# Kernel optimization log

Hardware: AMD Instinct MI355X
Metric: run time of the kernel (lower is better)

## Reference

```python
import math
import jax, jax.numpy as jnp
import numpy as np

HEAD_DIM = 64
N_HEAD = 8
INIT_SIZE = 1200  # -> 1201 embeddings, origin_shift = 601


def rel_sinusoidal_pos_embed(seq_len, dim=HEAD_DIM):
    """Matches RelativeSinusoidalPositionalEmbedding(dim, padding_idx=0, init_size=1200)."""
    num = INIT_SIZE + 1  # 1201
    half = dim // 2
    inv_freq = jnp.exp(jnp.arange(half, dtype=jnp.float32) * -(math.log(10000.0) / (half - 1)))
    pos = jnp.arange(-(num // 2), num // 2, dtype=jnp.float32)  # -601 .. 599 (1201 values)
    ang = pos[:, None] * inv_freq[None, :]                      # [num, half]
    w = jnp.concatenate([jnp.sin(ang), jnp.cos(ang)], axis=1)   # [num, dim]
    w = w.at[0].set(0.0)  # padding_idx row zeroed
    origin_shift = num // 2 + 1  # 601
    idx = jnp.arange(-seq_len, seq_len) + origin_shift          # [2L]
    return w[idx]                                               # [2L, dim]


def _shift(BD):
    # BD: [b, n, L, 2L] -> [b, n, L, L] (Transformer-XL skew trick)
    b, n, L, _ = BD.shape
    BD = jnp.pad(BD, ((0, 0), (0, 0), (0, 0), (0, 1)))  # [b,n,L,2L+1]
    BD = BD.reshape(b, n, 2 * L + 1, L)[:, :, :-1].reshape(b, n, L, 2 * L)
    return BD[:, :, :, L:]


def _transpose_shift(E):
    # E: [b, n, L, 2L] -> [b, n, L, L]
    b, n, L, _ = E.shape
    E = jnp.pad(E, ((0, 0), (0, 0), (0, 0), (0, 1))).reshape(b, n, 2 * L + 1, L)
    idx = jnp.arange(L) * 2 + 1
    return jnp.swapaxes(E[:, :, idx, :], -1, -2)


def setup_inputs() -> dict:
    key = jax.random.key(0)
    k1, k2, k3, k4 = jax.random.split(key, 4)
    B, L, D = 8, 512, 512
    x = jax.random.normal(k1, (B, L, D), dtype=jnp.float32)
    mask = jnp.ones((B, L), dtype=jnp.int32)
    W_qkv = jax.random.normal(k2, (D, 3 * D), dtype=jnp.float32) * (1.0 / math.sqrt(D))
    r_r_bias = jax.random.normal(k3, (N_HEAD, HEAD_DIM), dtype=jnp.float32) * 0.1
    r_w_bias = jax.random.normal(k4, (N_HEAD, HEAD_DIM), dtype=jnp.float32) * 0.1
    return {"x": x, "mask": mask, "W_qkv": W_qkv, "r_r_bias": r_r_bias, "r_w_bias": r_w_bias}


def reference(x, mask, W_qkv, r_r_bias, r_w_bias):
    B, L, D = x.shape
    scale = math.sqrt(HEAD_DIM)
    pos = rel_sinusoidal_pos_embed(L)  # [2L, head_dim], detached constant

    qkv = x @ W_qkv  # [B, L, 3D]
    q, k, v = jnp.split(qkv, 3, axis=-1)
    q = q.reshape(B, L, N_HEAD, HEAD_DIM).transpose(0, 2, 1, 3)  # [B,H,L,d]
    k = k.reshape(B, L, N_HEAD, HEAD_DIM).transpose(0, 2, 1, 3)
    v = v.reshape(B, L, N_HEAD, HEAD_DIM).transpose(0, 2, 1, 3)

    rw_head_q = q + r_r_bias[None, :, None, :]
    AC = jnp.einsum('bnqd,bnkd->bnqk', rw_head_q, k)              # [B,H,L,L]
    D_ = jnp.einsum('nd,ld->nl', r_w_bias, pos)[None, :, None, :] # [1,H,1,2L]
    B_ = jnp.einsum('bnqd,ld->bnql', q, pos)                      # [B,H,L,2L]
    E_ = jnp.einsum('bnqd,ld->bnql', k, pos)                      # [B,H,L,2L]

    BDE = _shift(B_ + D_) + _transpose_shift(E_)                  # [B,H,L,L]
    attn = (AC + BDE) / scale
    attn = jnp.where(mask[:, None, None, :] == 0, -jnp.inf, attn)
    attn = jax.nn.softmax(attn, axis=-1)

    out = jnp.matmul(attn, v)                                     # [B,H,L,d]
    return out.transpose(0, 2, 1, 3).reshape(B, L, D)
```

## Files before the change

kernel.cpp:

```cpp
#include <hip/hip_runtime.h>
#include <hip/hip_bf16.h>
#include <math.h>

#define LSEQ 512
#define DDIM 192

typedef __attribute__((ext_vector_type(8))) short s16x8;
typedef __attribute__((ext_vector_type(4))) float f32x4;
typedef unsigned short ushort_t;
typedef unsigned int uint_t;

#define MFMA16(a, b, c) __builtin_amdgcn_mfma_f32_16x16x32_bf16(a, b, c, 0, 0, 0)

__device__ __forceinline__ ushort_t f2b(float f) {
  union { float f; uint_t u; } v; v.f = f;
  uint_t r = (v.u + 0x7FFFu + ((v.u >> 16) & 1u)) >> 16;
  return (ushort_t)r;
}

typedef const __attribute__((address_space(1))) void g_void_t;
typedef __attribute__((address_space(3))) void lds_void_t;
__device__ __forceinline__ void load_lds16(const void* g, void* l) {
  __builtin_amdgcn_global_load_lds((g_void_t*)g, (lds_void_t*)l, 16, 0, 0);
}

__device__ __forceinline__ size_t kswz(size_t row, int d) {
  return row * DDIM + (size_t)((d & 0x1C7) | ((((d >> 3) & 7) ^ ((int)row & 7)) << 3));
}

__global__ void cast_all(const float* __restrict__ x, const float* __restrict__ W,
                         ushort_t* __restrict__ xb, ushort_t* __restrict__ Wt) {
  __shared__ float tile[32][33];
  const int id = blockIdx.x;
  if (id < 1024) {
    const int i = (id * 256 + threadIdx.x) * 8;
    const int row = i >> 9, k = i & 511;
    float4 a = *(const float4*)(x + i);
    float4 b = *(const float4*)(x + i + 4);
    uint4 o;
    o.x = (uint_t)f2b(a.x) | ((uint_t)f2b(a.y) << 16);
    o.y = (uint_t)f2b(a.z) | ((uint_t)f2b(a.w) << 16);
    o.z = (uint_t)f2b(b.x) | ((uint_t)f2b(b.y) << 16);
    o.w = (uint_t)f2b(b.z) | ((uint_t)f2b(b.w) << 16);
    const int dst = row * 512 + (k & 448) + (((((k >> 3) & 7) ^ (row & 7))) << 3);
    *(uint4*)(xb + dst) = o;
  } else {
    const int wid = id - 1024;
    const int tx = threadIdx.x & 31, ty = threadIdx.x >> 5;
    const int k0 = (wid & 15) * 32, n0 = (wid >> 4) * 32;
#pragma unroll
    for (int i = 0; i < 4; ++i)
      tile[ty + i * 8][tx] = W[(size_t)(k0 + ty + i * 8) * 1536 + n0 + tx];
    __syncthreads();
#pragma unroll
    for (int i = 0; i < 4; ++i) {
      const int n = n0 + ty + i * 8, k = k0 + tx;
      Wt[(size_t)n * 512 + (k & 448) + ((((k >> 3) & 7) ^ (n & 7)) << 3) + (k & 7)] =
          f2b(tile[tx][ty + i * 8]);
    }
  }
}

__global__ __launch_bounds__(256, 2) void qkv_gemm(
    const ushort_t* __restrict__ xb, const ushort_t* __restrict__ Wt,
    const float* __restrict__ rr, const float* __restrict__ rw,
    ushort_t* __restrict__ Qt, ushort_t* __restrict__ Kt, ushort_t* __restrict__ Vt) {
  __shared__ __align__(16) ushort_t ldsA[2][128 * 64];
  __shared__ __align__(16) ushort_t ldsB[2][128 * 64];
  const int tid = threadIdx.x;
  const int w = tid >> 6, lane = tid & 63, lo = lane & 15, hi = lane >> 4;
  const int wm = w >> 1, wn = w & 1;
  const int id = blockIdx.x;
  const int mp = id & 31, np = id >> 5;
  const int m0 = mp * 128, n0 = np * 128;

  f32x4 acc[4][4];
  const f32x4 zero4 = {0.f, 0.f, 0.f, 0.f};
#pragma unroll
  for (int i = 0; i < 4; ++i)
#pragma unroll
    for (int j = 0; j < 4; ++j) acc[i][j] = zero4;

  const char* asrc = (const char*)xb + (size_t)m0 * 1024;
  const char* bsrc = (const char*)Wt + (size_t)n0 * 1024;

#define STAGE_QKV(buf, ks)                                                     \
  {                                                                            \
    char* la = (char*)&ldsA[buf][0];                                           \
    char* lb = (char*)&ldsB[buf][0];                                           \
    _Pragma("unroll") for (int it = 0; it < 4; ++it) {                         \
      const int X = it * 4096 + tid * 16;                                      \
      load_lds16(asrc + (size_t)(X >> 7) * 1024 + (ks) * 128 + (X & 127),      \
                 la + X);                                                      \
      load_lds16(bsrc + (size_t)(X >> 7) * 1024 + (ks) * 128 + (X & 127),      \
                 lb + X);                                                      \
    }                                                                          \
  }

  STAGE_QKV(0, 0);
  for (int ks = 0; ks < 8; ++ks) {
    const int cur = ks & 1;
    __syncthreads();
    if (ks < 7) STAGE_QKV(cur ^ 1, ks + 1);
    const char* Ab = (const char*)&ldsA[cur][0];
    const char* Bb = (const char*)&ldsB[cur][0];
#pragma unroll
    for (int kh = 0; kh < 2; ++kh) {
      const int sw = ((kh * 4 + hi) ^ (lo & 7)) << 4;
      s16x8 a[4], bf[4];
#pragma unroll
      for (int i = 0; i < 4; ++i)
        a[i] = *(const s16x8*)(Ab + (wm * 64 + i * 16 + lo) * 128 + sw);
#pragma unroll
      for (int j = 0; j < 4; ++j)
        bf[j] = *(const s16x8*)(Bb + (wn * 64 + j * 16 + lo) * 128 + sw);
#pragma unroll
      for (int i = 0; i < 4; ++i)
#pragma unroll
        for (int j = 0; j < 4; ++j)
          acc[i][j] = MFMA16(a[i], bf[j], acc[i][j]);
    }
  }

  const int gn0 = n0 + wn * 64;
  const int sect = gn0 >> 9;
  const int h = (gn0 >> 6) & 7;
  const int mrow0 = m0 + wm * 64;

  if (sect == 2) {
#pragma unroll
    for (int i = 0; i < 4; ++i) {
      const int m16 = mrow0 + i * 16;
      const int b = m16 >> 9;
      const int l0 = (m16 + hi * 4) & 511;
#pragma unroll
      for (int j = 0; j < 4; ++j) {
        ushort4 pk;
        pk.x = f2b(acc[i][j][0]); pk.y = f2b(acc[i][j][1]);
        pk.z = f2b(acc[i][j][2]); pk.w = f2b(acc[i][j][3]);
        *(ushort4*)&Vt[(((size_t)b * 8 + h) * 64 + j * 16 + lo) * 512 + l0] = pk;
      }
    }
  } else if (sect == 0) {
#pragma unroll
    for (int p = 0; p < 2; ++p) {
      const int hf = p * 16 + lo;
      const float rrs = rr[h * 64 + hf], rrc = rr[h * 64 + 32 + hf];
      const float rws = rw[h * 64 + hf], rwc = rw[h * 64 + 32 + hf];
      const float fq = __expf(-(float)hf * 0.29710775393472f);
      float sfr, cfr;
      __sincosf(fq, &sfr, &cfr);
#pragma unroll
      for (int i = 0; i < 4; ++i)
#pragma unroll
        for (int r = 0; r < 4; ++r) {
          const int m = mrow0 + i * 16 + hi * 4 + r;
          const int l = m & 511;
          const size_t base = (((size_t)(m >> 9) * 8 + h) * 512 + l) * DDIM;
          float s0, c0;
          __sincosf((float)l * fq, &s0, &c0);
          const float s1 = s0 * cfr + c0 * sfr;
          const float c1 = c0 * cfr - s0 * sfr;
          const float vs = acc[i][p][r], vc = acc[i][p + 2][r];
          const float qs = (vs + rws) * 0.125f, qc = (vc + rwc) * 0.125f;
          Qt[base + hf]       = f2b((vs + rrs) * 0.125f);
          Qt[base + 32 + hf]  = f2b((vc + rrc) * 0.125f);
          Qt[base + 64 + hf]  = f2b(qs * c0 + qc * s0);
          Qt[base + 96 + hf]  = f2b(qc * c0 - qs * s0);
          Qt[base + 128 + hf] = f2b(0.125f * s1);
          Qt[base + 160 + hf] = f2b(0.125f * c1);
        }
    }
  } else {
#pragma unroll
    for (int p = 0; p < 2; ++p) {
      const int hf = p * 16 + lo;
      const float fq = __expf(-(float)hf * 0.29710775393472f);
      float sfr, cfr;
      __sincosf(fq, &sfr, &cfr);
#pragma unroll
      for (int i = 0; i < 4; ++i)
#pragma unroll
        for (int r = 0; r < 4; ++r) {
          const int m = mrow0 + i * 16 + hi * 4 + r;
          const int l = m & 511;
          const size_t row = ((size_t)(m >> 9) * 8 + h) * 512 + l;
          float s0, c0;
          __sincosf((float)l * fq, &s0, &c0);
          const float s1 = s0 * cfr + c0 * sfr;
          const float c1 = c0 * cfr - s0 * sfr;
          const float ks_ = acc[i][p][r], kc_ = acc[i][p + 2][r];
          Kt[kswz(row, hf)]       = f2b(ks_);
          Kt[kswz(row, 32 + hf)]  = f2b(kc_);
          Kt[kswz(row, 64 + hf)]  = f2b(s1);
          Kt[kswz(row, 96 + hf)]  = f2b(c1);
          Kt[kswz(row, 128 + hf)] = f2b(ks_ * c0 + kc_ * s0);
          Kt[kswz(row, 160 + hf)] = f2b(kc_ * c0 - ks_ * s0);
        }
    }
  }
}

__global__ __launch_bounds__(256, 2) void attn_kernel(
    const ushort_t* __restrict__ Qt, const ushort_t* __restrict__ Kt,
    const ushort_t* __restrict__ Vt, const int* __restrict__ mask,
    float* __restrict__ out) {
  __shared__ __align__(16) ushort_t ldsK[2][64 * DDIM];
  __shared__ __align__(16) ushort_t P[4][16][72];

  const int tid = threadIdx.x;
  const int w = tid >> 6;
  const int lane = tid & 63, lo = lane & 15, hi = lane >> 4;
  const int id = blockIdx.x;
  const int bh = id & 63, qg = id >> 6;
  const int b = bh >> 3, h = bh & 7;
  const int q0 = qg * 64 + w * 16;
  const size_t qrow0 = (size_t)bh * LSEQ + q0;

  s16x8 qf[6];
#pragma unroll
  for (int ks = 0; ks < 6; ++ks)
    qf[ks] = *(const s16x8*)(Qt + (qrow0 + lo) * DDIM + ks * 32 + hi * 8);

  const f32x4 zero4 = {0.f, 0.f, 0.f, 0.f};
  f32x4 o[4];
#pragma unroll
  for (int j = 0; j < 4; ++j) o[j] = zero4;
  float mrun = -3.0e38f, lrun = 0.f;

  const char* ksrc = (const char*)(Kt + (size_t)bh * LSEQ * DDIM);
  const ushort_t* vbase = Vt + ((size_t)bh * 64 + lo) * 512 + hi * 8;

#pragma unroll
  for (int it = 0; it < 6; ++it) {
    const int X = it * 4096 + tid * 16;
    load_lds16(ksrc + X, (char*)&ldsK[0][0] + X);
  }

  for (int kt = 0; kt < 8; ++kt) {
    const int cur = kt & 1;

    const int mk = mask[b * LSEQ + kt * 64 + lane];
    s16x8 vbf[2][4];
#pragma unroll
    for (int kh = 0; kh < 2; ++kh)
#pragma unroll
      for (int j = 0; j < 4; ++j)
        vbf[kh][j] = *(const s16x8*)(vbase + (size_t)j * 16 * 512 + kt * 64 + kh * 32);

    __syncthreads();
    if (kt < 7) {
      const char* s = ksrc + (kt + 1) * 24576;
      char* d = (char*)&ldsK[cur ^ 1][0];
#pragma unroll
      for (int it = 0; it < 6; ++it) {
        const int X = it * 4096 + tid * 16;
        load_lds16(s + X, d + X);
      }
    }

    f32x4 sf[4];
#pragma unroll
    for (int f = 0; f < 4; ++f) sf[f] = zero4;
    const char* kl = (const char*)&ldsK[cur][0];
    __builtin_amdgcn_s_setprio(1);
#pragma unroll
    for (int ks = 0; ks < 6; ++ks) {
      const int swb = ((ks * 4 + hi) ^ (lo & 7)) << 4;
#pragma unroll
      for (int f = 0; f < 4; ++f) {
        s16x8 ka = *(const s16x8*)(kl + (f * 16 + lo) * 384 + swb);
        sf[f] = MFMA16(ka, qf[ks], sf[f]);
      }
    }
    __builtin_amdgcn_s_setprio(0);

    if (__ballot(mk == 0) != 0ull) {
#pragma unroll
      for (int f = 0; f < 4; ++f)
#pragma unroll
        for (int r = 0; r < 4; ++r)
          if (__shfl(mk, f * 16 + hi * 4 + r) == 0) sf[f][r] = -3.0e38f;
    }

    float tm = fmaxf(fmaxf(sf[0][0], sf[0][1]), fmaxf(sf[0][2], sf[0][3]));
#pragma unroll
    for (int f = 1; f < 4; ++f)
      tm = fmaxf(tm, fmaxf(fmaxf(sf[f][0], sf[f][1]), fmaxf(sf[f][2], sf[f][3])));
    tm = fmaxf(tm, __shfl_xor(tm, 16));
    tm = fmaxf(tm, __shfl_xor(tm, 32));

    if (!__all(tm - mrun <= 8.0f)) {
      const float mnew = fmaxf(mrun, tm);
      const float corr = __expf(mrun - mnew);
      lrun *= corr;
      mrun = mnew;
      float cq[4];
#pragma unroll
      for (int r = 0; r < 4; ++r) cq[r] = __shfl(corr, hi * 4 + r);
#pragma unroll
      for (int j = 0; j < 4; ++j)
#pragma unroll
        for (int r = 0; r < 4; ++r) o[j][r] *= cq[r];
    }

    float ts = 0.f;
#pragma unroll
    for (int f = 0; f < 4; ++f)
#pragma unroll
      for (int r = 0; r < 4; ++r) {
        sf[f][r] = __expf(sf[f][r] - mrun);
        ts += sf[f][r];
      }
    ts += __shfl_xor(ts, 16);
    ts += __shfl_xor(ts, 32);
    lrun += ts;

#pragma unroll
    for (int f = 0; f < 4; ++f) {
      __hip_bfloat162 p0 = __float22bfloat162_rn(make_float2(sf[f][0], sf[f][1]));
      __hip_bfloat162 p1 = __float22bfloat162_rn(make_float2(sf[f][2], sf[f][3]));
      uint2 u;
      __builtin_memcpy(&u.x, &p0, 4);
      __builtin_memcpy(&u.y, &p1, 4);
      *(uint2*)&P[w][lo][f * 16 + hi * 4] = u;
    }

    __builtin_amdgcn_s_setprio(1);
#pragma unroll
    for (int kh = 0; kh < 2; ++kh) {
      s16x8 pa = *(const s16x8*)&P[w][lo][kh * 32 + hi * 8];
#pragma unroll
      for (int j = 0; j < 4; ++j)
        o[j] = MFMA16(pa, vbf[kh][j], o[j]);
    }
    __builtin_amdgcn_s_setprio(0);
  }

  float lq[4];
#pragma unroll
  for (int r = 0; r < 4; ++r) lq[r] = 1.0f / __shfl(lrun, hi * 4 + r);
#pragma unroll
  for (int j = 0; j < 4; ++j)
#pragma unroll
    for (int r = 0; r < 4; ++r)
      out[((size_t)b * LSEQ + q0 + hi * 4 + r) * 512 + h * 64 + j * 16 + lo] =
          o[j][r] * lq[r];
}

extern "C" void kernel_launch(void* const* d_in, const int* in_sizes, int n_in,
                              void* d_out, int out_size, void* d_ws, size_t ws_size,
                              hipStream_t stream) {
  const float* x    = (const float*)d_in[0];
  const int*   mask = (const int*)d_in[1];
  const float* W    = (const float*)d_in[2];
  const float* rr   = (const float*)d_in[3];
  const float* rw   = (const float*)d_in[4];
  float* out = (float*)d_out;

  char* ws = (char*)d_ws;
  ushort_t* xb = (ushort_t*)(ws);
  ushort_t* Wt = (ushort_t*)(ws + 4194304);
  ushort_t* Qt = (ushort_t*)(ws + 5767168);
  ushort_t* Kt = (ushort_t*)(ws + 18350080);
  ushort_t* Vt = (ushort_t*)(ws + 30932992);

  cast_all<<<1792, 256, 0, stream>>>(x, W, xb, Wt);
  qkv_gemm<<<384, 256, 0, stream>>>(xb, Wt, rr, rw, Qt, Kt, Vt);
  attn_kernel<<<512, 256, 0, stream>>>(Qt, Kt, Vt, mask, out);
}
```

Baseline: 53.35 us.

## Fuse cast, QKV GEMM and attention into one persistent kernel with grid barriers

Merges the three kernel launches into one 512-block persistent kernel. Its phases (cast, QKV GEMM, attention) are separated by atomic-counter grid barriers, and a tiny init kernel resets the counter each call. The aim is to remove launch gaps and inter-kernel drain/fill overhead. In exchange it relies on all 512 blocks being co-resident to avoid deadlock, adds spin-wait barrier costs, and uses a 64KB shared buffer that may limit occupancy. It also adds one extra small launch.

```diff
diff --git a/kernel.cpp b/kernel.cpp
--- a/kernel.cpp
+++ b/kernel.cpp
@@ -4,6 +4,7 @@
 
 #define LSEQ 512
 #define DDIM 192
+#define NBLK 512
 
 typedef __attribute__((ext_vector_type(8))) short s16x8;
 typedef __attribute__((ext_vector_type(4))) float f32x4;
@@ -28,66 +29,87 @@
   return row * DDIM + (size_t)((d & 0x1C7) | ((((d >> 3) & 7) ^ ((int)row & 7)) << 3));
 }
 
-__global__ void cast_all(const float* __restrict__ x, const float* __restrict__ W,
-                         ushort_t* __restrict__ xb, ushort_t* __restrict__ Wt) {
-  __shared__ float tile[32][33];
-  const int id = blockIdx.x;
-  if (id < 1024) {
-    const int i = (id * 256 + threadIdx.x) * 8;
-    const int row = i >> 9, k = i & 511;
-    float4 a = *(const float4*)(x + i);
-    float4 b = *(const float4*)(x + i + 4);
-    uint4 o;
-    o.x = (uint_t)f2b(a.x) | ((uint_t)f2b(a.y) << 16);
-    o.y = (uint_t)f2b(a.z) | ((uint_t)f2b(a.w) << 16);
-    o.z = (uint_t)f2b(b.x) | ((uint_t)f2b(b.y) << 16);
-    o.w = (uint_t)f2b(b.z) | ((uint_t)f2b(b.w) << 16);
-    const int dst = row * 512 + (k & 448) + (((((k >> 3) & 7) ^ (row & 7))) << 3);
-    *(uint4*)(xb + dst) = o;
-  } else {
-    const int wid = id - 1024;
-    const int tx = threadIdx.x & 31, ty = threadIdx.x >> 5;
-    const int k0 = (wid & 15) * 32, n0 = (wid >> 4) * 32;
+__global__ void init_bar(uint_t* c) { *c = 0u; }
+
+__device__ __forceinline__ void gridbar(uint_t* cnt, uint_t target) {
+  __syncthreads();
+  if (threadIdx.x == 0) {
+    __hip_atomic_fetch_add(cnt, 1u, __ATOMIC_ACQ_REL, __HIP_MEMORY_SCOPE_AGENT);
+    while (__hip_atomic_load(cnt, __ATOMIC_ACQUIRE, __HIP_MEMORY_SCOPE_AGENT) < target)
+      __builtin_amdgcn_s_sleep(2);
+  }
+  __syncthreads();
+}
+
+__global__ __launch_bounds__(256, 2) void mega(
+    const float* __restrict__ x, const float* __restrict__ W,
+    const float* __restrict__ rr, const float* __restrict__ rw,
+    const int* __restrict__ mask, float* __restrict__ out,
+    ushort_t* __restrict__ xb, ushort_t* __restrict__ Wt,
+    ushort_t* __restrict__ Qt, ushort_t* __restrict__ Kt,
+    ushort_t* __restrict__ Vt, uint_t* __restrict__ barcnt) {
+  __shared__ __align__(16) char smem[65536];
+  const int tid = threadIdx.x;
+  const int bid = blockIdx.x;
+
+  {
+    float (*tile)[33] = (float(*)[33])smem;
+    for (int unit = bid; unit < 1792; unit += NBLK) {
+      if (unit < 1024) {
+        const int i = (unit * 256 + tid) * 8;
+        const int row = i >> 9, k = i & 511;
+        float4 a = *(const float4*)(x + i);
+        float4 b = *(const float4*)(x + i + 4);
+        uint4 o;
+        o.x = (uint_t)f2b(a.x) | ((uint_t)f2b(a.y) << 16);
+        o.y = (uint_t)f2b(a.z) | ((uint_t)f2b(a.w) << 16);
+        o.z = (uint_t)f2b(b.x) | ((uint_t)f2b(b.y) << 16);
+        o.w = (uint_t)f2b(b.z) | ((uint_t)f2b(b.w) << 16);
+        const int dst = row * 512 + (k & 448) + (((((k >> 3) & 7) ^ (row & 7))) << 3);
+        *(uint4*)(xb + dst) = o;
+      } else {
+        const int wid = unit - 1024;
+        const int tx = tid & 31, ty = tid >> 5;
+        const int k0 = (wid & 15) * 32, n0 = (wid >> 4) * 32;
+        __syncthreads();
+#pragma unroll
+        for (int i = 0; i < 4; ++i)
+          tile[ty + i * 8][tx] = W[(size_t)(k0 + ty + i * 8) * 1536 + n0 + tx];
+        __syncthreads();
+#pragma unroll
+        for (int i = 0; i < 4; ++i) {
+          const int n = n0 + ty + i * 8, k = k0 + tx;
+          Wt[(size_t)n * 512 + (k & 448) + ((((k >> 3) & 7) ^ (n & 7)) << 3) + (k & 7)] =
+              f2b(tile[tx][ty + i * 8]);
+        }
+      }
+    }
+  }
+
+  gridbar(barcnt, NBLK);
+
+  if (bid < 384) {
+    ushort_t* ldsA = (ushort_t*)smem;
+    ushort_t* ldsB = (ushort_t*)(smem + 32768);
+    const int w = tid >> 6, lane = tid & 63, lo = lane & 15, hi = lane >> 4;
+    const int wm = w >> 1, wn = w & 1;
+    const int mp = bid & 31, np = bid >> 5;
+    const int m0 = mp * 128, n0 = np * 128;
+
+    f32x4 acc[4][4];
+    const f32x4 zero4 = {0.f, 0.f, 0.f, 0.f};
 #pragma unroll
     for (int i = 0; i < 4; ++i)
-      tile[ty + i * 8][tx] = W[(size_t)(k0 + ty + i * 8) * 1536 + n0 + tx];
-    __syncthreads();
-#pragma unroll
-    for (int i = 0; i < 4; ++i) {
-      const int n = n0 + ty + i * 8, k = k0 + tx;
-      Wt[(size_t)n * 512 + (k & 448) + ((((k >> 3) & 7) ^ (n & 7)) << 3) + (k & 7)] =
-          f2b(tile[tx][ty + i * 8]);
-    }
-  }
-}
-
-__global__ __launch_bounds__(256, 2) void qkv_gemm(
-    const ushort_t* __restrict__ xb, const ushort_t* __restrict__ Wt,
-    const float* __restrict__ rr, const float* __restrict__ rw,
-    ushort_t* __restrict__ Qt, ushort_t* __restrict__ Kt, ushort_t* __restrict__ Vt) {
-  __shared__ __align__(16) ushort_t ldsA[2][128 * 64];
-  __shared__ __align__(16) ushort_t ldsB[2][128 * 64];
-  const int tid = threadIdx.x;
-  const int w = tid >> 6, lane = tid & 63, lo = lane & 15, hi = lane >> 4;
-  const int wm = w >> 1, wn = w & 1;
-  const int id = blockIdx.x;
-  const int mp = id & 31, np = id >> 5;
-  const int m0 = mp * 128, n0 = np * 128;
-
-  f32x4 acc[4][4];
-  const f32x4 zero4 = {0.f, 0.f, 0.f, 0.f};
-#pragma unroll
-  for (int i = 0; i < 4; ++i)
-#pragma unroll
-    for (int j = 0; j < 4; ++j) acc[i][j] = zero4;
-
-  const char* asrc = (const char*)xb + (size_t)m0 * 1024;
-  const char* bsrc = (const char*)Wt + (size_t)n0 * 1024;
+#pragma unroll
+      for (int j = 0; j < 4; ++j) acc[i][j] = zero4;
+
+    const char* asrc = (const char*)xb + (size_t)m0 * 1024;
+    const char* bsrc = (const char*)Wt + (size_t)n0 * 1024;
 
 #define STAGE_QKV(buf, ks)                                                     \
   {                                                                            \
-    char* la = (char*)&ldsA[buf][0];                                           \
-    char* lb = (char*)&ldsB[buf][0];                                           \
+    char* la = (char*)ldsA + (buf) * 16384;                                    \
+    char* lb = (char*)ldsB + (buf) * 16384;                                    \
     _Pragma("unroll") for (int it = 0; it < 4; ++it) {                         \
       const int X = it * 4096 + tid * 16;                                      \
       load_lds16(asrc + (size_t)(X >> 7) * 1024 + (ks) * 128 + (X & 127),      \
@@ -97,255 +119,253 @@
     }                                                                          \
   }
 
-  STAGE_QKV(0, 0);
-  for (int ks = 0; ks < 8; ++ks) {
-    const int cur = ks & 1;
-    __syncthreads();
-    if (ks < 7) STAGE_QKV(cur ^ 1, ks + 1);
-    const char* Ab = (const char*)&ldsA[cur][0];
-    const char* Bb = (const char*)&ldsB[cur][0];
-#pragma unroll
-    for (int kh = 0; kh < 2; ++kh) {
-      const int sw = ((kh * 4 + hi) ^ (lo & 7)) << 4;
-      s16x8 a[4], bf[4];
-#pragma unroll
-      for (int i = 0; i < 4; ++i)
-        a[i] = *(const s16x8*)(Ab + (wm * 64 + i * 16 + lo) * 128 + sw);
-#pragma unroll
-      for (int j = 0; j < 4; ++j)
-        bf[j] = *(const s16x8*)(Bb + (wn * 64 + j * 16 + lo) * 128 + sw);
-#pragma unroll
-      for (int i = 0; i < 4; ++i)
+    STAGE_QKV(0, 0);
+    for (int ks = 0; ks < 8; ++ks) {
+      const int cur = ks & 1;
+      __syncthreads();
+      if (ks < 7) STAGE_QKV(cur ^ 1, ks + 1);
+      const char* Ab = (const char*)ldsA + cur * 16384;
+      const char* Bb = (const char*)ldsB + cur * 16384;
+#pragma unroll
+      for (int kh = 0; kh < 2; ++kh) {
+        const int sw = ((kh * 4 + hi) ^ (lo & 7)) << 4;
+        s16x8 a[4], bf[4];
+#pragma unroll
+        for (int i = 0; i < 4; ++i)
+          a[i] = *(const s16x8*)(Ab + (wm * 64 + i * 16 + lo) * 128 + sw);
 #pragma unroll
         for (int j = 0; j < 4; ++j)
-          acc[i][j] = MFMA16(a[i], bf[j], acc[i][j]);
-    }
-  }
-
-  const int gn0 = n0 + wn * 64;
-  const int sect = gn0 >> 9;
-  const int h = (gn0 >> 6) & 7;
-  const int mrow0 = m0 + wm * 64;
-
-  if (sect == 2) {
-#pragma unroll
-    for (int i = 0; i < 4; ++i) {
-      const int m16 = mrow0 + i * 16;
-      const int b = m16 >> 9;
-      const int l0 = (m16 + hi * 4) & 511;
-#pragma unroll
-      for (int j = 0; j < 4; ++j) {
-        ushort4 pk;
-        pk.x = f2b(acc[i][j][0]); pk.y = f2b(acc[i][j][1]);
-        pk.z = f2b(acc[i][j][2]); pk.w = f2b(acc[i][j][3]);
-        *(ushort4*)&Vt[(((size_t)b * 8 + h) * 64 + j * 16 + lo) * 512 + l0] = pk;
-      }
-    }
-  } else if (sect == 0) {
-#pragma unroll
-    for (int p = 0; p < 2; ++p) {
-      const int hf = p * 16 + lo;
-      const float rrs = rr[h * 64 + hf], rrc = rr[h * 64 + 32 + hf];
-      const float rws = rw[h * 64 + hf], rwc = rw[h * 64 + 32 + hf];
-      const float fq = __expf(-(float)hf * 0.29710775393472f);
-      float sfr, cfr;
-      __sincosf(fq, &sfr, &cfr);
-#pragma unroll
-      for (int i = 0; i < 4; ++i)
+          bf[j] = *(const s16x8*)(Bb + (wn * 64 + j * 16 + lo) * 128 + sw);
+#pragma unroll
+        for (int i = 0; i < 4; ++i)
+#pragma unroll
+          for (int j = 0; j < 4; ++j)
+            acc[i][j] = MFMA16(a[i], bf[j], acc[i][j]);
+      }
+    }
+
+    const int gn0 = n0 + wn * 64;
+    const int sect = gn0 >> 9;
+    const int h = (gn0 >> 6) & 7;
+    const int mrow0 = m0 + wm * 64;
+
+    if (sect == 2) {
+#pragma unroll
+      for (int i = 0; i < 4; ++i) {
+        const int m16 = mrow0 + i * 16;
+        const int b = m16 >> 9;
+        const int l0 = (m16 + hi * 4) & 511;
+#pragma unroll
+        for (int j = 0; j < 4; ++j) {
+          ushort4 pk;
+          pk.x = f2b(acc[i][j][0]); pk.y = f2b(acc[i][j][1]);
+          pk.z = f2b(acc[i][j][2]); pk.w = f2b(acc[i][j][3]);
+          *(ushort4*)&Vt[(((size_t)b * 8 + h) * 64 + j * 16 + lo) * 512 + l0] = pk;
+        }
+      }
+    } else if (sect == 0) {
+#pragma unroll
+      for (int p = 0; p < 2; ++p) {
+        const int hf = p * 16 + lo;
+        const float rrs = rr[h * 64 + hf], rrc = rr[h * 64 + 32 + hf];
+        const float rws = rw[h * 64 + hf], rwc = rw[h * 64 + 32 + hf];
+        const float fq = __expf(-(float)hf * 0.29710775393472f);
+        float sfr, cfr;
+        __sincosf(fq, &sfr, &cfr);
+#pragma unroll
+        for (int i = 0; i < 4; ++i)
+#pragma unroll
+          for (int r = 0; r < 4; ++r) {
+            const int m = mrow0 + i * 16 + hi * 4 + r;
+            const int l = m & 511;
+            const size_t base = (((size_t)(m >> 9) * 8 + h) * 512 + l) * DDIM;
+            float s0, c0;
+            __sincosf((float)l * fq, &s0, &c0);
+            const float s1 = s0 * cfr + c0 * sfr;
+            const float c1 = c0 * cfr - s0 * sfr;
+            const float vs = acc[i][p][r], vc = acc[i][p + 2][r];
+            const float qs = (vs + rws) * 0.125f, qc = (vc + rwc) * 0.125f;
+            Qt[base + hf]       = f2b((vs + rrs) * 0.125f);
+            Qt[base + 32 + hf]  = f2b((vc + rrc) * 0.125f);
+            Qt[base + 64 + hf]  = f2b(qs * c0 + qc * s0);
+            Qt[base + 96 + hf]  = f2b(qc * c0 - qs * s0);
+            Qt[base + 128 + hf] = f2b(0.125f * s1);
+            Qt[base + 160 + hf] = f2b(0.125f * c1);
+          }
+      }
+    } else {
+#pragma unroll
+      for (int p = 0; p < 2; ++p) {
+        const int hf = p * 16 + lo;
+        const float fq = __expf(-(float)hf * 0.29710775393472f);
+        float sfr, cfr;
+        __sincosf(fq, &sfr, &cfr);
+#pragma unroll
+        for (int i = 0; i < 4; ++i)
+#pragma unroll
+          for (int r = 0; r < 4; ++r) {
+            const int m = mrow0 + i * 16 + hi * 4 + r;
+            const int l = m & 511;
+            const size_t row = ((size_t)(m >> 9) * 8 + h) * 512 + l;
+            float s0, c0;
+            __sincosf((float)l * fq, &s0, &c0);
+            const float s1 = s0 * cfr + c0 * sfr;
+            const float c1 = c0 * cfr - s0 * sfr;
+            const float ks_ = acc[i][p][r], kc_ = acc[i][p + 2][r];
+            Kt[kswz(row, hf)]       = f2b(ks_);
+            Kt[kswz(row, 32 + hf)]  = f2b(kc_);
+            Kt[kswz(row, 64 + hf)]  = f2b(s1);
+            Kt[kswz(row, 96 + hf)]  = f2b(c1);
+            Kt[kswz(row, 128 + hf)] = f2b(ks_ * c0 + kc_ * s0);
+            Kt[kswz(row, 160 + hf)] = f2b(kc_ * c0 - ks_ * s0);
+          }
+      }
+    }
+  }
+
+  gridbar(barcnt, 2u * NBLK);
+
+  {
+    ushort_t* ldsK = (ushort_t*)smem;
+    ushort_t (*P)[16][72] = (ushort_t(*)[16][72])(smem + 49152);
+
+    const int w = tid >> 6;
+    const int lane = tid & 63, lo = lane & 15, hi = lane >> 4;
+    const int bh = bid & 63, qg = bid >> 6;
+    const int b = bh >> 3, h = bh & 7;
+    const int q0 = qg * 64 + w * 16;
+    const size_t qrow0 = (size_t)bh * LSEQ + q0;
+
+    s16x8 qf[6];
+#pragma unroll
+    for (int ks = 0; ks < 6; ++ks)
+      qf[ks] = *(const s16x8*)(Qt + (qrow0 + lo) * DDIM + ks * 32 + hi * 8);
+
+    const f32x4 zero4 = {0.f, 0.f, 0.f, 0.f};
+    f32x4 o[4];
+#pragma unroll
+    for (int j = 0; j < 4; ++j) o[j] = zero4;
+    float mrun = -3.0e38f, lrun = 0.f;
+
+    const char* ksrc = (const char*)(Kt + (size_t)bh * LSEQ * DDIM);
+    const ushort_t* vbase = Vt + ((size_t)bh * 64 + lo) * 512 + hi * 8;
+
+#pragma unroll
+    for (int it = 0; it < 6; ++it) {
+      const int X = it * 4096 + tid * 16;
+      load_lds16(ksrc + X, (char*)ldsK + X);
+    }
+
+    for (int kt = 0; kt < 8; ++kt) {
+      const int cur = kt & 1;
+
+      const int mk = mask[b * LSEQ + kt * 64 + lane];
+      s16x8 vbf[2][4];
+#pragma unroll
+      for (int kh = 0; kh < 2; ++kh)
+#pragma unroll
+        for (int j = 0; j < 4; ++j)
+          vbf[kh][j] = *(const s16x8*)(vbase + (size_t)j * 16 * 512 + kt * 64 + kh * 32);
+
+      __syncthreads();
+      if (kt < 7) {
+        const char* s = ksrc + (kt + 1) * 24576;
+        char* d = (char*)ldsK + (cur ^ 1) * 24576;
+#pragma unroll
+        for (int it = 0; it < 6; ++it) {
+          const int X = it * 4096 + tid * 16;
+          load_lds16(s + X, d + X);
+        }
+      }
+
+      f32x4 sf[4];
+#pragma unroll
+      for (int f = 0; f < 4; ++f) sf[f] = zero4;
+      const char* kl = (const char*)ldsK + cur * 24576;
+      __builtin_amdgcn_s_setprio(1);
+#pragma unroll
+      for (int ks = 0; ks < 6; ++ks) {
+        const int swb = ((ks * 4 + hi) ^ (lo & 7)) << 4;
+#pragma unroll
+        for (int f = 0; f < 4; ++f) {
+          s16x8 ka = *(const s16x8*)(kl + (f * 16 + lo) * 384 + swb);
+          sf[f] = MFMA16(ka, qf[ks], sf[f]);
+        }
+      }
+      __builtin_amdgcn_s_setprio(0);
+
+      if (__ballot(mk == 0) != 0ull) {
+#pragma unroll
+        for (int f = 0; f < 4; ++f)
+#pragma unroll
+          for (int r = 0; r < 4; ++r)
+            if (__shfl(mk, f * 16 + hi * 4 + r) == 0) sf[f][r] = -3.0e38f;
+      }
+
+      float tm = fmaxf(fmaxf(sf[0][0], sf[0][1]), fmaxf(sf[0][2], sf[0][3]));
+#pragma unroll
+      for (int f = 1; f < 4; ++f)
+        tm = fmaxf(tm, fmaxf(fmaxf(sf[f][0], sf[f][1]), fmaxf(sf[f][2], sf[f][3])));
+      tm = fmaxf(tm, __shfl_xor(tm, 16));
+      tm = fmaxf(tm, __shfl_xor(tm, 32));
+
+      if (!__all(tm - mrun <= 8.0f)) {
+        const float mnew = fmaxf(mrun, tm);
+        const float corr = __expf(mrun - mnew);
+        lrun *= corr;
+        mrun = mnew;
+        float cq[4];
+#pragma unroll
+        for (int r = 0; r < 4; ++r) cq[r] = __shfl(corr, hi * 4 + r);
+#pragma unroll
+        for (int j = 0; j < 4; ++j)
+#pragma unroll
+          for (int r = 0; r < 4; ++r) o[j][r] *= cq[r];
+      }
+
+      float ts = 0.f;
+#pragma unroll
+      for (int f = 0; f < 4; ++f)
 #pragma unroll
         for (int r = 0; r < 4; ++r) {
-          const int m = mrow0 + i * 16 + hi * 4 + r;
-          const int l = m & 511;
-          const size_t base = (((size_t)(m >> 9) * 8 + h) * 512 + l) * DDIM;
-          float s0, c0;
-          __sincosf((float)l * fq, &s0, &c0);
-          const float s1 = s0 * cfr + c0 * sfr;
-          const float c1 = c0 * cfr - s0 * sfr;
-          const float vs = acc[i][p][r], vc = acc[i][p + 2][r];
-          const float qs = (vs + rws) * 0.125f, qc = (vc + rwc) * 0.125f;
-          Qt[base + hf]       = f2b((vs + rrs) * 0.125f);
-          Qt[base + 32 + hf]  = f2b((vc + rrc) * 0.125f);
-          Qt[base + 64 + hf]  = f2b(qs * c0 + qc * s0);
-          Qt[base + 96 + hf]  = f2b(qc * c0 - qs * s0);
-          Qt[base + 128 + hf] = f2b(0.125f * s1);
-          Qt[base + 160 + hf] = f2b(0.125f * c1);
-        }
-    }
-  } else {
-#pragma unroll
-    for (int p = 0; p < 2; ++p) {
-      const int hf = p * 16 + lo;
-      const float fq = __expf(-(float)hf * 0.29710775393472f);
-      float sfr, cfr;
-      __sincosf(fq, &sfr, &cfr);
-#pragma unroll
-      for (int i = 0; i < 4; ++i)
-#pragma unroll
-        for (int r = 0; r < 4; ++r) {
-          const int m = mrow0 + i * 16 + hi * 4 + r;
-          const int l = m & 511;
-          const size_t row = ((size_t)(m >> 9) * 8 + h) * 512 + l;
-          float s0, c0;
-          __sincosf((float)l * fq, &s0, &c0);
-          const float s1 = s0 * cfr + c0 * sfr;
-          const float c1 = c0 * cfr - s0 * sfr;
-          const float ks_ = acc[i][p][r], kc_ = acc[i][p + 2][r];
-          Kt[kswz(row, hf)]       = f2b(ks_);
-          Kt[kswz(row, 32 + hf)]  = f2b(kc_);
-          Kt[kswz(row, 64 + hf)]  = f2b(s1);
-          Kt[kswz(row, 96 + hf)]  = f2b(c1);
-          Kt[kswz(row, 128 + hf)] = f2b(ks_ * c0 + kc_ * s0);
-          Kt[kswz(row, 160 + hf)] = f2b(kc_ * c0 - ks_ * s0);
-        }
-    }
-  }
-}
-
-__global__ __launch_bounds__(256, 2) void attn_kernel(
-    const ushort_t* __restrict__ Qt, const ushort_t* __restrict__ Kt,
-    const ushort_t* __restrict__ Vt, const int* __restrict__ mask,
-    float* __restrict__ out) {
-  __shared__ __align__(16) ushort_t ldsK[2][64 * DDIM];
-  __shared__ __align__(16) ushort_t P[4][16][72];
-
-  const int tid = threadIdx.x;
-  const int w = tid >> 6;
-  const int lane = tid & 63, lo = lane & 15, hi = lane >> 4;
-  const int id = blockIdx.x;
-  const int bh = id & 63, qg = id >> 6;
-  const int b = bh >> 3, h = bh & 7;
-  const int q0 = qg * 64 + w * 16;
-  const size_t qrow0 = (size_t)bh * LSEQ + q0;
-
-  s16x8 qf[6];
-#pragma unroll
-  for (int ks = 0; ks < 6; ++ks)
-    qf[ks] = *(const s16x8*)(Qt + (qrow0 + lo) * DDIM + ks * 32 + hi * 8);
-
-  const f32x4 zero4 = {0.f, 0.f, 0.f, 0.f};
-  f32x4 o[4];
-#pragma unroll
-  for (int j = 0; j < 4; ++j) o[j] = zero4;
-  float mrun = -3.0e38f, lrun = 0.f;
-
-  const char* ksrc = (const char*)(Kt + (size_t)bh * LSEQ * DDIM);
-  const ushort_t* vbase = Vt + ((size_t)bh * 64 + lo) * 512 + hi * 8;
-
-#pragma unroll
-  for (int it = 0; it < 6; ++it) {
-    const int X = it * 4096 + tid * 16;
-    load_lds16(ksrc + X, (char*)&ldsK[0][0] + X);
-  }
-
-  for (int kt = 0; kt < 8; ++kt) {
-    const int cur = kt & 1;
-
-    const int mk = mask[b * LSEQ + kt * 64 + lane];
-    s16x8 vbf[2][4];
-#pragma unroll
-    for (int kh = 0; kh < 2; ++kh)
-#pragma unroll
-      for (int j = 0; j < 4; ++j)
-        vbf[kh][j] = *(const s16x8*)(vbase + (size_t)j * 16 * 512 + kt * 64 + kh * 32);
-
-    __syncthreads();
-    if (kt < 7) {
-      const char* s = ksrc + (kt + 1) * 24576;
-      char* d = (char*)&ldsK[cur ^ 1][0];
-#pragma unroll
-      for (int it = 0; it < 6; ++it) {
-        const int X = it * 4096 + tid * 16;
-        load_lds16(s + X, d + X);
-      }
-    }
-
-    f32x4 sf[4];
-#pragma unroll
-    for (int f = 0; f < 4; ++f) sf[f] = zero4;
-    const char* kl = (const char*)&ldsK[cur][0];
-    __builtin_amdgcn_s_setprio(1);
-#pragma unroll
-    for (int ks = 0; ks < 6; ++ks) {
-      const int swb = ((ks * 4 + hi) ^ (lo & 7)) << 4;
+          sf[f][r] = __expf(sf[f][r] - mrun);
+          ts += sf[f][r];
+        }
+      ts += __shfl_xor(ts, 16);
+      ts += __shfl_xor(ts, 32);
+      lrun += ts;
+
 #pragma unroll
       for (int f = 0; f < 4; ++f) {
-        s16x8 ka = *(const s16x8*)(kl + (f * 16 + lo) * 384 + swb);
-        sf[f] = MFMA16(ka, qf[ks], sf[f]);
-      }
-    }
-    __builtin_amdgcn_s_setprio(0);
-
-    if (__ballot(mk == 0) != 0ull) {
-#pragma unroll
-      for (int f = 0; f < 4; ++f)
-#pragma unroll
-        for (int r = 0; r < 4; ++r)
-          if (__shfl(mk, f * 16 + hi * 4 + r) == 0) sf[f][r] = -3.0e38f;
-    }
-
-    float tm = fmaxf(fmaxf(sf[0][0], sf[0][1]), fmaxf(sf[0][2], sf[0][3]));
-#pragma unroll
-    for (int f = 1; f < 4; ++f)
-      tm = fmaxf(tm, fmaxf(fmaxf(sf[f][0], sf[f][1]), fmaxf(sf[f][2], sf[f][3])));
-    tm = fmaxf(tm, __shfl_xor(tm, 16));
-    tm = fmaxf(tm, __shfl_xor(tm, 32));
-
-    if (!__all(tm - mrun <= 8.0f)) {
-      const float mnew = fmaxf(mrun, tm);
-      const float corr = __expf(mrun - mnew);
-      lrun *= corr;
-      mrun = mnew;
-      float cq[4];
-#pragma unroll
-      for (int r = 0; r < 4; ++r) cq[r] = __shfl(corr, hi * 4 + r);
-#pragma unroll
-      for (int j = 0; j < 4; ++j)
-#pragma unroll
-        for (int r = 0; r < 4; ++r) o[j][r] *= cq[r];
-    }
-
-    float ts = 0.f;
-#pragma unroll
-    for (int f = 0; f < 4; ++f)
-#pragma unroll
-      for (int r = 0; r < 4; ++r) {
-        sf[f][r] = __expf(sf[f][r] - mrun);
-        ts += sf[f][r];
-      }
-    ts += __shfl_xor(ts, 16);
-    ts += __shfl_xor(ts, 32);
-    lrun += ts;
-
-#pragma unroll
-    for (int f = 0; f < 4; ++f) {
-      __hip_bfloat162 p0 = __float22bfloat162_rn(make_float2(sf[f][0], sf[f][1]));
-      __hip_bfloat162 p1 = __float22bfloat162_rn(make_float2(sf[f][2], sf[f][3]));
-      uint2 u;
-      __builtin_memcpy(&u.x, &p0, 4);
-      __builtin_memcpy(&u.y, &p1, 4);
-      *(uint2*)&P[w][lo][f * 16 + hi * 4] = u;
-    }
-
-    __builtin_amdgcn_s_setprio(1);
-#pragma unroll
-    for (int kh = 0; kh < 2; ++kh) {
-      s16x8 pa = *(const s16x8*)&P[w][lo][kh * 32 + hi * 8];
-#pragma unroll
-      for (int j = 0; j < 4; ++j)
-        o[j] = MFMA16(pa, vbf[kh][j], o[j]);
-    }
-    __builtin_amdgcn_s_setprio(0);
-  }
-
-  float lq[4];
-#pragma unroll
-  for (int r = 0; r < 4; ++r) lq[r] = 1.0f / __shfl(lrun, hi * 4 + r);
-#pragma unroll
-  for (int j = 0; j < 4; ++j)
-#pragma unroll
-    for (int r = 0; r < 4; ++r)
-      out[((size_t)b * LSEQ + q0 + hi * 4 + r) * 512 + h * 64 + j * 16 + lo] =
-          o[j][r] * lq[r];
+        __hip_bfloat162 p0 = __float22bfloat162_rn(make_float2(sf[f][0], sf[f][1]));
+        __hip_bfloat162 p1 = __float22bfloat162_rn(make_float2(sf[f][2], sf[f][3]));
+        uint2 u;
+        __builtin_memcpy(&u.x, &p0, 4);
+        __builtin_memcpy(&u.y, &p1, 4);
+        *(uint2*)&P[w][lo][f * 16 + hi * 4] = u;
+      }
+
+      __builtin_amdgcn_s_setprio(1);
+#pragma unroll
+      for (int kh = 0; kh < 2; ++kh) {
+        s16x8 pa = *(const s16x8*)&P[w][lo][kh * 32 + hi * 8];
+#pragma unroll
+        for (int j = 0; j < 4; ++j)
+          o[j] = MFMA16(pa, vbf[kh][j], o[j]);
+      }
+      __builtin_amdgcn_s_setprio(0);
+    }
+
+    float lq[4];
+#pragma unroll
+    for (int r = 0; r < 4; ++r) lq[r] = 1.0f / __shfl(lrun, hi * 4 + r);
+#pragma unroll
+    for (int j = 0; j < 4; ++j)
+#pragma unroll
+      for (int r = 0; r < 4; ++r)
+        out[((size_t)b * LSEQ + q0 + hi * 4 + r) * 512 + h * 64 + j * 16 + lo] =
+            o[j][r] * lq[r];
+  }
 }
 
 extern "C" void kernel_launch(void* const* d_in, const int* in_sizes, int n_in,
@@ -364,8 +384,8 @@
   ushort_t* Qt = (ushort_t*)(ws + 5767168);
   ushort_t* Kt = (ushort_t*)(ws + 18350080);
   ushort_t* Vt = (ushort_t*)(ws + 30932992);
-
-  cast_all<<<1792, 256, 0, stream>>>(x, W, xb, Wt);
-  qkv_gemm<<<384, 256, 0, stream>>>(xb, Wt, rr, rw, Qt, Kt, Vt);
-  attn_kernel<<<512, 256, 0, stream>>>(Qt, Kt, Vt, mask, out);
-}
+  uint_t* barcnt = (uint_t*)(ws + 35651584);
+
+  init_bar<<<1, 1, 0, stream>>>(barcnt);
+  mega<<<NBLK, 256, 0, stream>>>(x, W, rr, rw, mask, out, xb, Wt, Qt, Kt, Vt, barcnt);
+}
```

After: 172.0 us. 222% more time.

## Store only 64-wide biased Q and rebuild rotated Q features inside attention

Applied to the files above, without the earlier changes.

The QKV GEMM epilogue now writes only the 64 biased Q columns instead of a 192-wide augmented Q row. The attention kernel reconstructs the rotated positional columns and the sinusoid columns from that compact Q plus the bias difference, computed in registers at load time. This cuts Q write and read traffic by about two thirds at the cost of extra transcendental math per thread. It also replaces __syncthreads with a partial vmcnt wait plus a barrier, so the V register loads can stay in flight across the barrier. Q is double-rounded through bf16 before the rotation, which adds a little error.

```diff
diff --git a/kernel.cpp b/kernel.cpp
--- a/kernel.cpp
+++ b/kernel.cpp
@@ -16,6 +16,10 @@
   union { float f; uint_t u; } v; v.f = f;
   uint_t r = (v.u + 0x7FFFu + ((v.u >> 16) & 1u)) >> 16;
   return (ushort_t)r;
+}
+__device__ __forceinline__ float b2f(ushort_t u) {
+  union { uint_t u; float f; } v; v.u = ((uint_t)u) << 16;
+  return v.f;
 }
 
 typedef const __attribute__((address_space(1))) void g_void_t;
@@ -142,35 +146,23 @@
       }
     }
   } else if (sect == 0) {
-#pragma unroll
-    for (int p = 0; p < 2; ++p) {
-      const int hf = p * 16 + lo;
-      const float rrs = rr[h * 64 + hf], rrc = rr[h * 64 + 32 + hf];
-      const float rws = rw[h * 64 + hf], rwc = rw[h * 64 + 32 + hf];
-      const float fq = __expf(-(float)hf * 0.29710775393472f);
-      float sfr, cfr;
-      __sincosf(fq, &sfr, &cfr);
-#pragma unroll
-      for (int i = 0; i < 4; ++i)
-#pragma unroll
-        for (int r = 0; r < 4; ++r) {
-          const int m = mrow0 + i * 16 + hi * 4 + r;
-          const int l = m & 511;
-          const size_t base = (((size_t)(m >> 9) * 8 + h) * 512 + l) * DDIM;
-          float s0, c0;
-          __sincosf((float)l * fq, &s0, &c0);
-          const float s1 = s0 * cfr + c0 * sfr;
-          const float c1 = c0 * cfr - s0 * sfr;
-          const float vs = acc[i][p][r], vc = acc[i][p + 2][r];
-          const float qs = (vs + rws) * 0.125f, qc = (vc + rwc) * 0.125f;
-          Qt[base + hf]       = f2b((vs + rrs) * 0.125f);
-          Qt[base + 32 + hf]  = f2b((vc + rrc) * 0.125f);
-          Qt[base + 64 + hf]  = f2b(qs * c0 + qc * s0);
-          Qt[base + 96 + hf]  = f2b(qc * c0 - qs * s0);
-          Qt[base + 128 + hf] = f2b(0.125f * s1);
-          Qt[base + 160 + hf] = f2b(0.125f * c1);
-        }
-    }
+    float bias[4];
+    int dcol[4];
+#pragma unroll
+    for (int j = 0; j < 4; ++j) {
+      dcol[j] = (j < 2) ? j * 16 + lo : 32 + (j - 2) * 16 + lo;
+      bias[j] = rr[h * 64 + dcol[j]];
+    }
+#pragma unroll
+    for (int i = 0; i < 4; ++i)
+#pragma unroll
+      for (int r = 0; r < 4; ++r) {
+        const int m = mrow0 + i * 16 + hi * 4 + r;
+        const size_t row = ((size_t)(m >> 9) * 8 + h) * 512 + (m & 511);
+#pragma unroll
+        for (int j = 0; j < 4; ++j)
+          Qt[row * 64 + dcol[j]] = f2b((acc[i][j][r] + bias[j]) * 0.125f);
+      }
   } else {
 #pragma unroll
     for (int p = 0; p < 2; ++p) {
@@ -204,6 +196,7 @@
 __global__ __launch_bounds__(256, 2) void attn_kernel(
     const ushort_t* __restrict__ Qt, const ushort_t* __restrict__ Kt,
     const ushort_t* __restrict__ Vt, const int* __restrict__ mask,
+    const float* __restrict__ rr, const float* __restrict__ rw,
     float* __restrict__ out) {
   __shared__ __align__(16) ushort_t ldsK[2][64 * DDIM];
   __shared__ __align__(16) ushort_t P[4][16][72];
@@ -218,9 +211,28 @@
   const size_t qrow0 = (size_t)bh * LSEQ + q0;
 
   s16x8 qf[6];
-#pragma unroll
-  for (int ks = 0; ks < 6; ++ks)
-    qf[ks] = *(const s16x8*)(Qt + (qrow0 + lo) * DDIM + ks * 32 + hi * 8);
+  {
+    const ushort_t* qbase = Qt + (qrow0 + lo) * 64 + hi * 8;
+    qf[0] = *(const s16x8*)(qbase);
+    qf[1] = *(const s16x8*)(qbase + 32);
+    const int l = q0 + lo;
+#pragma unroll
+    for (int j = 0; j < 8; ++j) {
+      const int hfj = hi * 8 + j;
+      const float fq = __expf(-(float)hfj * 0.29710775393472f);
+      float s0, c0, s1, c1;
+      __sincosf((float)l * fq, &s0, &c0);
+      __sincosf((float)(l + 1) * fq, &s1, &c1);
+      const float ds = 0.125f * (rw[h * 64 + hfj] - rr[h * 64 + hfj]);
+      const float dc = 0.125f * (rw[h * 64 + 32 + hfj] - rr[h * 64 + 32 + hfj]);
+      const float qs = b2f((ushort_t)qf[0][j]) + ds;
+      const float qc = b2f((ushort_t)qf[1][j]) + dc;
+      qf[2][j] = (short)f2b(qs * c0 + qc * s0);
+      qf[3][j] = (short)f2b(qc * c0 - qs * s0);
+      qf[4][j] = (short)f2b(0.125f * s1);
+      qf[5][j] = (short)f2b(0.125f * c1);
+    }
+  }
 
   const f32x4 zero4 = {0.f, 0.f, 0.f, 0.f};
   f32x4 o[4];
@@ -248,7 +260,10 @@
       for (int j = 0; j < 4; ++j)
         vbf[kh][j] = *(const s16x8*)(vbase + (size_t)j * 16 * 512 + kt * 64 + kh * 32);
 
-    __syncthreads();
+    asm volatile("s_waitcnt vmcnt(8)" ::: "memory");
+    __builtin_amdgcn_s_barrier();
+    __builtin_amdgcn_sched_barrier(0);
+
     if (kt < 7) {
       const char* s = ksrc + (kt + 1) * 24576;
       char* d = (char*)&ldsK[cur ^ 1][0];
@@ -362,10 +377,10 @@
   ushort_t* xb = (ushort_t*)(ws);
   ushort_t* Wt = (ushort_t*)(ws + 4194304);
   ushort_t* Qt = (ushort_t*)(ws + 5767168);
-  ushort_t* Kt = (ushort_t*)(ws + 18350080);
-  ushort_t* Vt = (ushort_t*)(ws + 30932992);
+  ushort_t* Kt = (ushort_t*)(ws + 9961472);
+  ushort_t* Vt = (ushort_t*)(ws + 22544384);
 
   cast_all<<<1792, 256, 0, stream>>>(x, W, xb, Wt);
   qkv_gemm<<<384, 256, 0, stream>>>(xb, Wt, rr, rw, Qt, Kt, Vt);
-  attn_kernel<<<512, 256, 0, stream>>>(Qt, Kt, Vt, mask, out);
-}
+  attn_kernel<<<512, 256, 0, stream>>>(Qt, Kt, Vt, mask, rr, rw, out);
+}
```

Measured after the change: 51.33 us. 3.8% less time.
